# Optimization experiments

Hardware: AMD Instinct MI355X
Metric: run time of the kernel (lower is better)

Reference implementation:

```python
import jax, jax.numpy as jnp
import numpy as np

TOPK = 2


def setup_inputs() -> dict:
    key = jax.random.key(0)
    k0, k1, k2, k3, k4 = jax.random.split(key, 5)
    B, S, D, E, H = 4, 2048, 1024, 8, 2816
    return {
        "x": jax.random.normal(k0, (B, S, D), dtype=jnp.float32),
        "gate_w": jax.random.normal(k1, (E, D), dtype=jnp.float32) * 0.02,
        "w1": jax.random.normal(k2, (E, H, D), dtype=jnp.float32) * 0.02,
        "w2": jax.random.normal(k3, (E, D, H), dtype=jnp.float32) * 0.02,
        "w3": jax.random.normal(k4, (E, H, D), dtype=jnp.float32) * 0.02,
    }


def reference(x, gate_w, w1, w2, w3):
    B, S, D = x.shape
    E = gate_w.shape[0]
    T = B * S
    xf = x.reshape(T, D)

    # Router: top-k logits, softmax over the selected k, scatter into a
    # dense [T, E] combine-weight matrix (equivalent to the index_add combine).
    logits = xf @ gate_w.T                      # [T, E]
    tw, ti = jax.lax.top_k(logits, TOPK)        # [T, k]
    tw = jax.nn.softmax(tw, axis=-1)
    cw = jnp.zeros((T, E), dtype=xf.dtype).at[
        jnp.arange(T)[:, None], ti
    ].add(tw)                                   # [T, E] combine weights

    # Expert SwiGLU FFNs, combined with routing weights. Loop over the small
    # fixed expert count; tokens with cw==0 contribute zero, matching the
    # masked dispatch in the original module.
    out = jnp.zeros_like(xf)
    for e in range(E):
        h = jax.nn.silu(xf @ w1[e].T) * (xf @ w3[e].T)   # [T, H]
        out = out + cw[:, e:e + 1] * (h @ w2[e].T)       # [T, D]
    return out.reshape(B, S, D)
```

## Files before the change

kernel.cpp:

```cpp
#include <hip/hip_runtime.h>
#include <stdint.h>

#define T_TOK 8192
#define DIM   1024
#define NEXP  8
#define HID   2816

typedef __bf16 bf16x8 __attribute__((ext_vector_type(8)));
typedef float  f32x4  __attribute__((ext_vector_type(4)));

typedef __attribute__((address_space(3))) uint32_t lds_u32_t;
typedef __attribute__((address_space(1))) const uint32_t gbl_u32_t;

__device__ __forceinline__ void gl_lds16(const void* g, void* l) {
    __builtin_amdgcn_global_load_lds((gbl_u32_t*)g, (lds_u32_t*)l, 16, 0, 0);
}

__device__ __forceinline__ uint32_t f2bf_u(float f) {
    uint32_t u = __builtin_bit_cast(uint32_t, f);
    return u + 0x7fffu + ((u >> 16) & 1u);
}
__device__ __forceinline__ uint32_t pack2(float a, float b) {
    return (f2bf_u(a) >> 16) | (f2bf_u(b) & 0xffff0000u);
}

__global__ __launch_bounds__(256) void cvt_k(
    const float* __restrict__ s, unsigned short* __restrict__ d, int n8)
{
    int i = blockIdx.x * 256 + threadIdx.x;
    if (i < n8) {
        const float4* sp = (const float4*)(s + (size_t)i * 8);
        float4 a = sp[0], b = sp[1];
        uint4 o;
        o.x = pack2(a.x, a.y); o.y = pack2(a.z, a.w);
        o.z = pack2(b.x, b.y); o.w = pack2(b.z, b.w);
        ((uint4*)d)[i] = o;
    }
}

__global__ __launch_bounds__(256) void router_k(
    const float* __restrict__ x, const float* __restrict__ gw,
    int* __restrict__ cnt, int* __restrict__ slot_list,
    float* __restrict__ slot_w)
{
    const int wave = threadIdx.x >> 6, lane = threadIdx.x & 63;
    const int t = blockIdx.x * 4 + wave;
    const float4* xp = (const float4*)(x + (size_t)t * DIM + lane * 16);
    float4 xv[4];
#pragma unroll
    for (int i = 0; i < 4; ++i) xv[i] = xp[i];

    double lg[NEXP];
#pragma unroll
    for (int e = 0; e < NEXP; ++e) {
        const float4* gp = (const float4*)(gw + (size_t)e * DIM + lane * 16);
        double s = 0.0;
#pragma unroll
        for (int i = 0; i < 4; ++i) {
            float4 g = gp[i];
            s += (double)xv[i].x * g.x + (double)xv[i].y * g.y +
                 (double)xv[i].z * g.z + (double)xv[i].w * g.w;
        }
#pragma unroll
        for (int m = 32; m >= 1; m >>= 1) s += __shfl_xor(s, m, 64);
        lg[e] = s;
    }

    if (lane == 0) {
        int e0 = 0; double b0 = lg[0];
#pragma unroll
        for (int e = 1; e < NEXP; ++e)
            if (lg[e] > b0) { b0 = lg[e]; e0 = e; }
        int e1 = -1; double b1 = -1.0e300;
#pragma unroll
        for (int e = 0; e < NEXP; ++e)
            if (e != e0 && lg[e] > b1) { b1 = lg[e]; e1 = e; }

        float p0 = (float)(1.0 / (1.0 + exp(b1 - b0)));
        float p1 = 1.0f - p0;

        int pos0 = atomicAdd(&cnt[e0], 1);
        slot_list[e0 * T_TOK + pos0] = 2 * t;
        slot_w[2 * t] = p0;
        int pos1 = atomicAdd(&cnt[e1], 1);
        slot_list[e1 * T_TOK + pos1] = 2 * t + 1;
        slot_w[2 * t + 1] = p1;
    }
}

__global__ __launch_bounds__(256) void ffn1_k(
    const unsigned short* __restrict__ xb, const unsigned short* __restrict__ w1b,
    const unsigned short* __restrict__ w3b, const int* __restrict__ cnt,
    const int* __restrict__ slot_list, unsigned short* __restrict__ h_ws)
{
    __shared__ unsigned short As[128 * 32];
    __shared__ unsigned short B1s[64 * 32];
    __shared__ unsigned short B2s[64 * 32];
    __shared__ int slots_s[128];

    const int e = blockIdx.z;
    const int cntE = cnt[e];
    const int m0 = blockIdx.y * 128;
    if (m0 >= cntE) return;
    const int n0 = blockIdx.x * 64;
    const int tid = threadIdx.x;
    const int wave = tid >> 6, lane = tid & 63;

    if (tid < 128) {
        int idx = m0 + tid;
        slots_s[tid] = (idx < cntE) ? slot_list[e * T_TOK + idx] : -1;
    }
    __syncthreads();

    const int sub = lane >> 2;
    const int kq  = lane & 3;
    const unsigned short* gsrc[4];
    unsigned short* ldst[4];
    if (wave < 2) {
#pragma unroll
        for (int i = 0; i < 4; ++i) {
            int row = wave * 64 + i * 16 + sub;
            int slot = slots_s[row];
            int tok = (slot >= 0) ? (slot >> 1) : 0;
            gsrc[i] = xb + (size_t)tok * DIM + kq * 8;
            ldst[i] = &As[(wave * 64 + i * 16) * 32];
        }
    } else if (wave == 2) {
#pragma unroll
        for (int i = 0; i < 4; ++i) {
            int row = i * 16 + sub;
            gsrc[i] = w1b + ((size_t)e * HID + n0 + row) * DIM + kq * 8;
            ldst[i] = &B1s[(i * 16) * 32];
        }
    } else {
#pragma unroll
        for (int i = 0; i < 4; ++i) {
            int row = i * 16 + sub;
            gsrc[i] = w3b + ((size_t)e * HID + n0 + row) * DIM + kq * 8;
            ldst[i] = &B2s[(i * 16) * 32];
        }
    }

    const int wm = wave >> 1, wn = wave & 1;
    const int lrow = lane & 15, koff = (lane >> 4) * 8, quad = lane >> 4;

    f32x4 acc1[4][2], acc2[4][2];
    const f32x4 zf = {0.f, 0.f, 0.f, 0.f};
#pragma unroll
    for (int mi = 0; mi < 4; ++mi)
#pragma unroll
        for (int ni = 0; ni < 2; ++ni) { acc1[mi][ni] = zf; acc2[mi][ni] = zf; }

    for (int k0 = 0; k0 < DIM; k0 += 32) {
#pragma unroll
        for (int i = 0; i < 4; ++i) gl_lds16(gsrc[i], ldst[i]);
#pragma unroll
        for (int i = 0; i < 4; ++i) gsrc[i] += 32;
        __syncthreads();

        bf16x8 af[4], b1f[2], b2f[2];
#pragma unroll
        for (int mi = 0; mi < 4; ++mi)
            af[mi] = *(const bf16x8*)&As[(wm * 64 + mi * 16 + lrow) * 32 + koff];
#pragma unroll
        for (int ni = 0; ni < 2; ++ni) {
            b1f[ni] = *(const bf16x8*)&B1s[(wn * 32 + ni * 16 + lrow) * 32 + koff];
            b2f[ni] = *(const bf16x8*)&B2s[(wn * 32 + ni * 16 + lrow) * 32 + koff];
        }
#pragma unroll
        for (int mi = 0; mi < 4; ++mi)
#pragma unroll
            for (int ni = 0; ni < 2; ++ni) {
                acc1[mi][ni] = __builtin_amdgcn_mfma_f32_16x16x32_bf16(
                    af[mi], b1f[ni], acc1[mi][ni], 0, 0, 0);
                acc2[mi][ni] = __builtin_amdgcn_mfma_f32_16x16x32_bf16(
                    af[mi], b2f[ni], acc2[mi][ni], 0, 0, 0);
            }
        __syncthreads();
    }

#pragma unroll
    for (int mi = 0; mi < 4; ++mi) {
#pragma unroll
        for (int r = 0; r < 4; ++r) {
            int mloc = wm * 64 + mi * 16 + quad * 4 + r;
            int slot = slots_s[mloc];
            if (slot >= 0) {
                unsigned short* hrow =
                    h_ws + (size_t)slot * HID + n0 + wn * 32 + lrow;
#pragma unroll
                for (int ni = 0; ni < 2; ++ni) {
                    float a1 = acc1[mi][ni][r], a3 = acc2[mi][ni][r];
                    float hv = (a1 / (1.f + __expf(-a1))) * a3;
                    hrow[ni * 16] = (unsigned short)(f2bf_u(hv) >> 16);
                }
            }
        }
    }
}

__global__ __launch_bounds__(256) void ffn2_k(
    const unsigned short* __restrict__ h_ws, const unsigned short* __restrict__ w2b,
    const int* __restrict__ cnt, const int* __restrict__ slot_list,
    const float* __restrict__ slot_w, float* __restrict__ out)
{
    __shared__ unsigned short As[128 * 32];
    __shared__ unsigned short Bs[128 * 32];
    __shared__ int slots_s[128];
    __shared__ float wgt_s[128];

    const int e = blockIdx.z;
    const int cntE = cnt[e];
    const int m0 = blockIdx.y * 128;
    if (m0 >= cntE) return;
    const int n0 = blockIdx.x * 128;
    const int tid = threadIdx.x;
    const int wave = tid >> 6, lane = tid & 63;

    if (tid < 128) {
        int idx = m0 + tid;
        int s = (idx < cntE) ? slot_list[e * T_TOK + idx] : -1;
        slots_s[tid] = s;
        wgt_s[tid] = (s >= 0) ? slot_w[s] : 0.f;
    }
    __syncthreads();

    const int sub = lane >> 2, kq = lane & 3;
    const unsigned short* gsrc[4];
    unsigned short* ldst[4];
    if (wave < 2) {
#pragma unroll
        for (int i = 0; i < 4; ++i) {
            int row = wave * 64 + i * 16 + sub;
            int slot = slots_s[row];
            int s = (slot >= 0) ? slot : 0;
            gsrc[i] = h_ws + (size_t)s * HID + kq * 8;
            ldst[i] = &As[(wave * 64 + i * 16) * 32];
        }
    } else {
#pragma unroll
        for (int i = 0; i < 4; ++i) {
            int row = (wave - 2) * 64 + i * 16 + sub;
            gsrc[i] = w2b + ((size_t)e * DIM + n0 + row) * HID + kq * 8;
            ldst[i] = &Bs[((wave - 2) * 64 + i * 16) * 32];
        }
    }

    const int wm = wave >> 1, wn = wave & 1;
    const int lrow = lane & 15, koff = (lane >> 4) * 8, quad = lane >> 4;

    f32x4 acc[4][4];
    const f32x4 zf = {0.f, 0.f, 0.f, 0.f};
#pragma unroll
    for (int mi = 0; mi < 4; ++mi)
#pragma unroll
        for (int ni = 0; ni < 4; ++ni) acc[mi][ni] = zf;

    for (int k0 = 0; k0 < HID; k0 += 32) {
#pragma unroll
        for (int i = 0; i < 4; ++i) gl_lds16(gsrc[i], ldst[i]);
#pragma unroll
        for (int i = 0; i < 4; ++i) gsrc[i] += 32;
        __syncthreads();

        bf16x8 af[4], bf[4];
#pragma unroll
        for (int mi = 0; mi < 4; ++mi)
            af[mi] = *(const bf16x8*)&As[(wm * 64 + mi * 16 + lrow) * 32 + koff];
#pragma unroll
        for (int ni = 0; ni < 4; ++ni)
            bf[ni] = *(const bf16x8*)&Bs[(wn * 64 + ni * 16 + lrow) * 32 + koff];
#pragma unroll
        for (int mi = 0; mi < 4; ++mi)
#pragma unroll
            for (int ni = 0; ni < 4; ++ni)
                acc[mi][ni] = __builtin_amdgcn_mfma_f32_16x16x32_bf16(
                    af[mi], bf[ni], acc[mi][ni], 0, 0, 0);
        __syncthreads();
    }

#pragma unroll
    for (int mi = 0; mi < 4; ++mi) {
#pragma unroll
        for (int r = 0; r < 4; ++r) {
            int mloc = wm * 64 + mi * 16 + quad * 4 + r;
            int slot = slots_s[mloc];
            if (slot >= 0) {
                int tok = slot >> 1;
                float w = wgt_s[mloc];
                float* orow = out + (size_t)tok * DIM + n0 + wn * 64 + lrow;
#pragma unroll
                for (int ni = 0; ni < 4; ++ni)
                    atomicAdd(&orow[ni * 16], acc[mi][ni][r] * w);
            }
        }
    }
}

extern "C" void kernel_launch(void* const* d_in, const int* in_sizes, int n_in,
                              void* d_out, int out_size, void* d_ws, size_t ws_size,
                              hipStream_t stream) {
    const float* x  = (const float*)d_in[0];
    const float* gw = (const float*)d_in[1];
    const float* w1 = (const float*)d_in[2];
    const float* w2 = (const float*)d_in[3];
    const float* w3 = (const float*)d_in[4];
    float* out = (float*)d_out;

    char* ws = (char*)d_ws;
    int*   cnt       = (int*)ws;
    int*   slot_list = (int*)(ws + 256);
    float* slot_w    = (float*)(ws + 256 + NEXP * T_TOK * 4);
    unsigned short* h_ws = (unsigned short*)(ws + 327936);
    unsigned short* x_bf = (unsigned short*)(ws + 92602624);
    unsigned short* w1_bf = (unsigned short*)(ws + 109379840);
    unsigned short* w3_bf = (unsigned short*)(ws + 155517184);
    unsigned short* w2_bf = (unsigned short*)(ws + 201654528);

    hipMemsetAsync(cnt, 0, 256, stream);
    hipMemsetAsync(out, 0, (size_t)T_TOK * DIM * sizeof(float), stream);

    const int nx = T_TOK * DIM / 8;
    const int nw = NEXP * HID * DIM / 8;
    cvt_k<<<(nx + 255) / 256, 256, 0, stream>>>(x, x_bf, nx);
    cvt_k<<<(nw + 255) / 256, 256, 0, stream>>>(w1, w1_bf, nw);
    cvt_k<<<(nw + 255) / 256, 256, 0, stream>>>(w3, w3_bf, nw);
    cvt_k<<<(nw + 255) / 256, 256, 0, stream>>>(w2, w2_bf, nw);

    router_k<<<T_TOK / 4, 256, 0, stream>>>(x, gw, cnt, slot_list, slot_w);
    ffn1_k<<<dim3(HID / 64, T_TOK / 128, NEXP), 256, 0, stream>>>(
        x_bf, w1_bf, w3_bf, cnt, slot_list, h_ws);
    ffn2_k<<<dim3(DIM / 128, T_TOK / 128, NEXP), 256, 0, stream>>>(
        h_ws, w2_bf, cnt, slot_list, slot_w, out);
}
```

Before: 939.7 us.

## Double K tile with XOR-swizzled LDS, replace output atomics with combine pass

Both expert GEMM kernels now stage 64-wide K slices instead of 32. The LDS layout is XOR-swizzled so the 16-byte fragment reads avoid bank conflicts, and barriers per K step are halved. The second FFN kernel writes weighted per-slot results to a scratch buffer instead of doing float atomicAdds into the output. A new combine kernel sums the two slots per token, which removes the output memset. The three weight conversions are merged into one launch, and the scratch buffer reuses the dead w1/w3 bf16 region at the cost of an extra 64MB write and read.

```diff
diff --git a/kernel.cpp b/kernel.cpp
--- a/kernel.cpp
+++ b/kernel.cpp
@@ -38,6 +38,25 @@
     }
 }
 
+__global__ __launch_bounds__(256) void cvt3_k(
+    const float* __restrict__ s1, const float* __restrict__ s3,
+    const float* __restrict__ s2, unsigned short* __restrict__ d1,
+    unsigned short* __restrict__ d3, unsigned short* __restrict__ d2, int n8)
+{
+    int i = blockIdx.x * 256 + threadIdx.x;
+    if (i >= n8) return;
+    const float* s; unsigned short* d;
+    if (blockIdx.y == 0)      { s = s1; d = d1; }
+    else if (blockIdx.y == 1) { s = s3; d = d3; }
+    else                      { s = s2; d = d2; }
+    const float4* sp = (const float4*)(s + (size_t)i * 8);
+    float4 a = sp[0], b = sp[1];
+    uint4 o;
+    o.x = pack2(a.x, a.y); o.y = pack2(a.z, a.w);
+    o.z = pack2(b.x, b.y); o.w = pack2(b.z, b.w);
+    ((uint4*)d)[i] = o;
+}
+
 __global__ __launch_bounds__(256) void router_k(
     const float* __restrict__ x, const float* __restrict__ gw,
     int* __restrict__ cnt, int* __restrict__ slot_list,
@@ -93,9 +112,9 @@
     const unsigned short* __restrict__ w3b, const int* __restrict__ cnt,
     const int* __restrict__ slot_list, unsigned short* __restrict__ h_ws)
 {
-    __shared__ unsigned short As[128 * 32];
-    __shared__ unsigned short B1s[64 * 32];
-    __shared__ unsigned short B2s[64 * 32];
+    __shared__ unsigned short As[128 * 64];
+    __shared__ unsigned short B1s[64 * 64];
+    __shared__ unsigned short B2s[64 * 64];
     __shared__ int slots_s[128];
 
     const int e = blockIdx.z;
@@ -112,37 +131,40 @@
     }
     __syncthreads();
 
-    const int sub = lane >> 2;
-    const int kq  = lane & 3;
-    const unsigned short* gsrc[4];
-    unsigned short* ldst[4];
+    const int sub = lane >> 3;
+    const int kq  = lane & 7;
+    const int qg  = kq ^ sub;
+    const unsigned short* gsrc[8];
+    unsigned short* ldst[8];
     if (wave < 2) {
 #pragma unroll
-        for (int i = 0; i < 4; ++i) {
-            int row = wave * 64 + i * 16 + sub;
+        for (int i = 0; i < 8; ++i) {
+            int row = wave * 64 + i * 8 + sub;
             int slot = slots_s[row];
             int tok = (slot >= 0) ? (slot >> 1) : 0;
-            gsrc[i] = xb + (size_t)tok * DIM + kq * 8;
-            ldst[i] = &As[(wave * 64 + i * 16) * 32];
+            gsrc[i] = xb + (size_t)tok * DIM + qg * 8;
+            ldst[i] = &As[(wave * 64 + i * 8) * 64];
         }
     } else if (wave == 2) {
 #pragma unroll
-        for (int i = 0; i < 4; ++i) {
-            int row = i * 16 + sub;
-            gsrc[i] = w1b + ((size_t)e * HID + n0 + row) * DIM + kq * 8;
-            ldst[i] = &B1s[(i * 16) * 32];
+        for (int i = 0; i < 8; ++i) {
+            int row = i * 8 + sub;
+            gsrc[i] = w1b + ((size_t)e * HID + n0 + row) * DIM + qg * 8;
+            ldst[i] = &B1s[(i * 8) * 64];
         }
     } else {
 #pragma unroll
-        for (int i = 0; i < 4; ++i) {
-            int row = i * 16 + sub;
-            gsrc[i] = w3b + ((size_t)e * HID + n0 + row) * DIM + kq * 8;
-            ldst[i] = &B2s[(i * 16) * 32];
+        for (int i = 0; i < 8; ++i) {
+            int row = i * 8 + sub;
+            gsrc[i] = w3b + ((size_t)e * HID + n0 + row) * DIM + qg * 8;
+            ldst[i] = &B2s[(i * 8) * 64];
         }
     }
 
     const int wm = wave >> 1, wn = wave & 1;
-    const int lrow = lane & 15, koff = (lane >> 4) * 8, quad = lane >> 4;
+    const int lrow = lane & 15, quad = lane >> 4;
+    const int s_r = lrow & 7;
+    const int ko[2] = { (quad ^ s_r) * 8, ((quad | 4) ^ s_r) * 8 };
 
     f32x4 acc1[4][2], acc2[4][2];
     const f32x4 zf = {0.f, 0.f, 0.f, 0.f};
@@ -151,31 +173,34 @@
 #pragma unroll
         for (int ni = 0; ni < 2; ++ni) { acc1[mi][ni] = zf; acc2[mi][ni] = zf; }
 
-    for (int k0 = 0; k0 < DIM; k0 += 32) {
-#pragma unroll
-        for (int i = 0; i < 4; ++i) gl_lds16(gsrc[i], ldst[i]);
-#pragma unroll
-        for (int i = 0; i < 4; ++i) gsrc[i] += 32;
+    for (int k0 = 0; k0 < DIM; k0 += 64) {
+#pragma unroll
+        for (int i = 0; i < 8; ++i) gl_lds16(gsrc[i], ldst[i]);
+#pragma unroll
+        for (int i = 0; i < 8; ++i) gsrc[i] += 64;
         __syncthreads();
 
-        bf16x8 af[4], b1f[2], b2f[2];
-#pragma unroll
-        for (int mi = 0; mi < 4; ++mi)
-            af[mi] = *(const bf16x8*)&As[(wm * 64 + mi * 16 + lrow) * 32 + koff];
-#pragma unroll
-        for (int ni = 0; ni < 2; ++ni) {
-            b1f[ni] = *(const bf16x8*)&B1s[(wn * 32 + ni * 16 + lrow) * 32 + koff];
-            b2f[ni] = *(const bf16x8*)&B2s[(wn * 32 + ni * 16 + lrow) * 32 + koff];
-        }
-#pragma unroll
-        for (int mi = 0; mi < 4; ++mi)
+#pragma unroll
+        for (int kh = 0; kh < 2; ++kh) {
+            bf16x8 af[4], b1f[2], b2f[2];
+#pragma unroll
+            for (int mi = 0; mi < 4; ++mi)
+                af[mi] = *(const bf16x8*)&As[(wm * 64 + mi * 16 + lrow) * 64 + ko[kh]];
 #pragma unroll
             for (int ni = 0; ni < 2; ++ni) {
-                acc1[mi][ni] = __builtin_amdgcn_mfma_f32_16x16x32_bf16(
-                    af[mi], b1f[ni], acc1[mi][ni], 0, 0, 0);
-                acc2[mi][ni] = __builtin_amdgcn_mfma_f32_16x16x32_bf16(
-                    af[mi], b2f[ni], acc2[mi][ni], 0, 0, 0);
+                b1f[ni] = *(const bf16x8*)&B1s[(wn * 32 + ni * 16 + lrow) * 64 + ko[kh]];
+                b2f[ni] = *(const bf16x8*)&B2s[(wn * 32 + ni * 16 + lrow) * 64 + ko[kh]];
             }
+#pragma unroll
+            for (int mi = 0; mi < 4; ++mi)
+#pragma unroll
+                for (int ni = 0; ni < 2; ++ni) {
+                    acc1[mi][ni] = __builtin_amdgcn_mfma_f32_16x16x32_bf16(
+                        af[mi], b1f[ni], acc1[mi][ni], 0, 0, 0);
+                    acc2[mi][ni] = __builtin_amdgcn_mfma_f32_16x16x32_bf16(
+                        af[mi], b2f[ni], acc2[mi][ni], 0, 0, 0);
+                }
+        }
         __syncthreads();
     }
 
@@ -202,10 +227,10 @@
 __global__ __launch_bounds__(256) void ffn2_k(
     const unsigned short* __restrict__ h_ws, const unsigned short* __restrict__ w2b,
     const int* __restrict__ cnt, const int* __restrict__ slot_list,
-    const float* __restrict__ slot_w, float* __restrict__ out)
-{
-    __shared__ unsigned short As[128 * 32];
-    __shared__ unsigned short Bs[128 * 32];
+    const float* __restrict__ slot_w, float* __restrict__ y_ws)
+{
+    __shared__ unsigned short As[128 * 64];
+    __shared__ unsigned short Bs[128 * 64];
     __shared__ int slots_s[128];
     __shared__ float wgt_s[128];
 
@@ -225,29 +250,32 @@
     }
     __syncthreads();
 
-    const int sub = lane >> 2, kq = lane & 3;
-    const unsigned short* gsrc[4];
-    unsigned short* ldst[4];
+    const int sub = lane >> 3, kq = lane & 7;
+    const int qg = kq ^ sub;
+    const unsigned short* gsrc[8];
+    unsigned short* ldst[8];
     if (wave < 2) {
 #pragma unroll
-        for (int i = 0; i < 4; ++i) {
-            int row = wave * 64 + i * 16 + sub;
+        for (int i = 0; i < 8; ++i) {
+            int row = wave * 64 + i * 8 + sub;
             int slot = slots_s[row];
             int s = (slot >= 0) ? slot : 0;
-            gsrc[i] = h_ws + (size_t)s * HID + kq * 8;
-            ldst[i] = &As[(wave * 64 + i * 16) * 32];
+            gsrc[i] = h_ws + (size_t)s * HID + qg * 8;
+            ldst[i] = &As[(wave * 64 + i * 8) * 64];
         }
     } else {
 #pragma unroll
-        for (int i = 0; i < 4; ++i) {
-            int row = (wave - 2) * 64 + i * 16 + sub;
-            gsrc[i] = w2b + ((size_t)e * DIM + n0 + row) * HID + kq * 8;
-            ldst[i] = &Bs[((wave - 2) * 64 + i * 16) * 32];
+        for (int i = 0; i < 8; ++i) {
+            int row = (wave - 2) * 64 + i * 8 + sub;
+            gsrc[i] = w2b + ((size_t)e * DIM + n0 + row) * HID + qg * 8;
+            ldst[i] = &Bs[((wave - 2) * 64 + i * 8) * 64];
         }
     }
 
     const int wm = wave >> 1, wn = wave & 1;
-    const int lrow = lane & 15, koff = (lane >> 4) * 8, quad = lane >> 4;
+    const int lrow = lane & 15, quad = lane >> 4;
+    const int s_r = lrow & 7;
+    const int ko[2] = { (quad ^ s_r) * 8, ((quad | 4) ^ s_r) * 8 };
 
     f32x4 acc[4][4];
     const f32x4 zf = {0.f, 0.f, 0.f, 0.f};
@@ -256,26 +284,29 @@
 #pragma unroll
         for (int ni = 0; ni < 4; ++ni) acc[mi][ni] = zf;
 
-    for (int k0 = 0; k0 < HID; k0 += 32) {
-#pragma unroll
-        for (int i = 0; i < 4; ++i) gl_lds16(gsrc[i], ldst[i]);
-#pragma unroll
-        for (int i = 0; i < 4; ++i) gsrc[i] += 32;
+    for (int k0 = 0; k0 < HID; k0 += 64) {
+#pragma unroll
+        for (int i = 0; i < 8; ++i) gl_lds16(gsrc[i], ldst[i]);
+#pragma unroll
+        for (int i = 0; i < 8; ++i) gsrc[i] += 64;
         __syncthreads();
 
-        bf16x8 af[4], bf[4];
-#pragma unroll
-        for (int mi = 0; mi < 4; ++mi)
-            af[mi] = *(const bf16x8*)&As[(wm * 64 + mi * 16 + lrow) * 32 + koff];
-#pragma unroll
-        for (int ni = 0; ni < 4; ++ni)
-            bf[ni] = *(const bf16x8*)&Bs[(wn * 64 + ni * 16 + lrow) * 32 + koff];
-#pragma unroll
-        for (int mi = 0; mi < 4; ++mi)
+#pragma unroll
+        for (int kh = 0; kh < 2; ++kh) {
+            bf16x8 af[4], bf[4];
+#pragma unroll
+            for (int mi = 0; mi < 4; ++mi)
+                af[mi] = *(const bf16x8*)&As[(wm * 64 + mi * 16 + lrow) * 64 + ko[kh]];
 #pragma unroll
             for (int ni = 0; ni < 4; ++ni)
-                acc[mi][ni] = __builtin_amdgcn_mfma_f32_16x16x32_bf16(
-                    af[mi], bf[ni], acc[mi][ni], 0, 0, 0);
+                bf[ni] = *(const bf16x8*)&Bs[(wn * 64 + ni * 16 + lrow) * 64 + ko[kh]];
+#pragma unroll
+            for (int mi = 0; mi < 4; ++mi)
+#pragma unroll
+                for (int ni = 0; ni < 4; ++ni)
+                    acc[mi][ni] = __builtin_amdgcn_mfma_f32_16x16x32_bf16(
+                        af[mi], bf[ni], acc[mi][ni], 0, 0, 0);
+        }
         __syncthreads();
     }
 
@@ -286,15 +317,25 @@
             int mloc = wm * 64 + mi * 16 + quad * 4 + r;
             int slot = slots_s[mloc];
             if (slot >= 0) {
-                int tok = slot >> 1;
                 float w = wgt_s[mloc];
-                float* orow = out + (size_t)tok * DIM + n0 + wn * 64 + lrow;
+                float* yrow = y_ws + (size_t)slot * DIM + n0 + wn * 64 + lrow;
 #pragma unroll
                 for (int ni = 0; ni < 4; ++ni)
-                    atomicAdd(&orow[ni * 16], acc[mi][ni][r] * w);
+                    yrow[ni * 16] = acc[mi][ni][r] * w;
             }
         }
     }
+}
+
+__global__ __launch_bounds__(256) void combine_k(
+    const float* __restrict__ y_ws, float* __restrict__ out)
+{
+    const int t = blockIdx.x, i = threadIdx.x;
+    const float4* a = (const float4*)(y_ws + (size_t)(2 * t) * DIM);
+    const float4* b = (const float4*)(y_ws + (size_t)(2 * t + 1) * DIM);
+    float4 va = a[i], vb = b[i];
+    float4 o = { va.x + vb.x, va.y + vb.y, va.z + vb.z, va.w + vb.w };
+    ((float4*)(out + (size_t)t * DIM))[i] = o;
 }
 
 extern "C" void kernel_launch(void* const* d_in, const int* in_sizes, int n_in,
@@ -311,25 +352,25 @@
     int*   cnt       = (int*)ws;
     int*   slot_list = (int*)(ws + 256);
     float* slot_w    = (float*)(ws + 256 + NEXP * T_TOK * 4);
-    unsigned short* h_ws = (unsigned short*)(ws + 327936);
-    unsigned short* x_bf = (unsigned short*)(ws + 92602624);
+    unsigned short* h_ws  = (unsigned short*)(ws + 327936);
+    unsigned short* x_bf  = (unsigned short*)(ws + 92602624);
     unsigned short* w1_bf = (unsigned short*)(ws + 109379840);
     unsigned short* w3_bf = (unsigned short*)(ws + 155517184);
     unsigned short* w2_bf = (unsigned short*)(ws + 201654528);
+    float* y_ws = (float*)(ws + 109379840);
 
     hipMemsetAsync(cnt, 0, 256, stream);
-    hipMemsetAsync(out, 0, (size_t)T_TOK * DIM * sizeof(float), stream);
 
     const int nx = T_TOK * DIM / 8;
     const int nw = NEXP * HID * DIM / 8;
     cvt_k<<<(nx + 255) / 256, 256, 0, stream>>>(x, x_bf, nx);
-    cvt_k<<<(nw + 255) / 256, 256, 0, stream>>>(w1, w1_bf, nw);
-    cvt_k<<<(nw + 255) / 256, 256, 0, stream>>>(w3, w3_bf, nw);
-    cvt_k<<<(nw + 255) / 256, 256, 0, stream>>>(w2, w2_bf, nw);
+    cvt3_k<<<dim3((nw + 255) / 256, 3), 256, 0, stream>>>(
+        w1, w3, w2, w1_bf, w3_bf, w2_bf, nw);
 
     router_k<<<T_TOK / 4, 256, 0, stream>>>(x, gw, cnt, slot_list, slot_w);
     ffn1_k<<<dim3(HID / 64, T_TOK / 128, NEXP), 256, 0, stream>>>(
         x_bf, w1_bf, w3_bf, cnt, slot_list, h_ws);
     ffn2_k<<<dim3(DIM / 128, T_TOK / 128, NEXP), 256, 0, stream>>>(
-        h_ws, w2_bf, cnt, slot_list, slot_w, out);
-}
+        h_ws, w2_bf, cnt, slot_list, slot_w, y_ws);
+    combine_k<<<T_TOK, 256, 0, stream>>>(y_ws, out);
+}
```

Result: slower. 961.2 us (+2.3%).
